# Performance work log

Measured on AMD Instinct MI355X. Metric: run time of the kernel, lower is better.

The kernel has to match this reference:

```python
import jax, jax.numpy as jnp
import numpy as np

TAU = 1.0
EPS_LN = 1e-5


def setup_inputs() -> dict:
    key = jax.random.key(0)
    ks = jax.random.split(key, 6)
    B, D, C, E, H = 32768, 768, 474, 3, 128
    x = jax.random.normal(ks[0], (B, D), dtype=jnp.float32)
    # pre-sampled uniform -> gumbel noise happens in reference; here store standard
    # gumbel noise directly (equivalent distribution to -log(-log(U)))
    u = jax.random.uniform(ks[1], (B, E), dtype=jnp.float32)
    gumbel_noise = -jnp.log(-jnp.log(u + 1e-20) + 1e-20)
    sel_w1 = jax.random.normal(ks[2], (D, H), dtype=jnp.float32) * (1.0 / np.sqrt(D))
    sel_b1 = jnp.zeros((H,), dtype=jnp.float32)
    sel_w2 = jax.random.normal(ks[3], (H, E), dtype=jnp.float32) * (1.0 / np.sqrt(H))
    sel_b2 = jnp.zeros((E,), dtype=jnp.float32)
    ln_gamma = jnp.ones((E, D), dtype=jnp.float32)
    ln_beta = jnp.zeros((E, D), dtype=jnp.float32)
    head_w = jax.random.normal(ks[4], (E, D, C), dtype=jnp.float32) * (1.0 / np.sqrt(D))
    head_b = jnp.zeros((E, C), dtype=jnp.float32)
    return {"x": x, "gumbel_noise": gumbel_noise, "sel_w1": sel_w1, "sel_b1": sel_b1,
            "sel_w2": sel_w2, "sel_b2": sel_b2, "ln_gamma": ln_gamma, "ln_beta": ln_beta,
            "head_w": head_w, "head_b": head_b}


def reference(x, gumbel_noise, sel_w1, sel_b1, sel_w2, sel_b2,
              ln_gamma, ln_beta, head_w, head_b):
    # selector MLP: Linear(768,128) -> ReLU -> Linear(128,3)
    h = jax.nn.relu(x @ sel_w1 + sel_b1)
    logits = h @ sel_w2 + sel_b2                       # [B, 3]

    # hard gumbel-softmax with straight-through estimator
    y = jax.nn.softmax((logits + gumbel_noise) / TAU, axis=-1)
    y_hard = jax.nn.one_hot(jnp.argmax(y, axis=-1), y.shape[-1], dtype=y.dtype)
    selection = jax.lax.stop_gradient(y_hard - y) + y  # [B, 3]

    # 3 expert heads: LayerNorm(768) -> Linear(768,474); dropout is identity (eval)
    mu = jnp.mean(x, axis=-1, keepdims=True)
    var = jnp.mean((x - mu) ** 2, axis=-1, keepdims=True)
    xn = (x - mu) * jax.lax.rsqrt(var + EPS_LN)        # [B, D]
    xs = xn[:, None, :] * ln_gamma[None] + ln_beta[None]   # [B, 3, D]
    outputs = jnp.einsum('bed,edc->bec', xs, head_w) + head_b  # [B, 3, C]

    # mask-and-sum combine
    return jnp.sum(outputs * selection[:, :, None], axis=1)    # [B, C]
```

## Files before the change

### kernel.cpp

```cpp
#include <hip/hip_runtime.h>
#include <hip/hip_bf16.h>
#include <math.h>

#define NB 32768
#define ND 768
#define NC 474
#define NCP 512
#define NE 3
#define NH 128
#define GAP_THR 0.035f
#define XB_OFF 4194304ull

typedef short v8s __attribute__((ext_vector_type(8)));
typedef float v4f __attribute__((ext_vector_type(4)));
typedef unsigned long long u64;

#define GLD16(gp, lp) __builtin_amdgcn_global_load_lds( \
    (const __attribute__((address_space(1))) void*)(gp), \
    (__attribute__((address_space(3))) void*)(lp), 16, 0, 0)

static __device__ __forceinline__ short f2bf(float f) {
    __hip_bfloat16 h = __float2bfloat16(f);
    return *reinterpret_cast<short*>(&h);
}

static __device__ __forceinline__ void vmwait(int n) {
    switch (n) {
    case 0:  asm volatile("s_waitcnt vmcnt(0)"  ::: "memory"); break;
    case 5:  asm volatile("s_waitcnt vmcnt(5)"  ::: "memory"); break;
    case 6:  asm volatile("s_waitcnt vmcnt(6)"  ::: "memory"); break;
    case 12: asm volatile("s_waitcnt vmcnt(12)" ::: "memory"); break;
    default: asm volatile("s_waitcnt vmcnt(10)" ::: "memory"); break;
    }
}

__global__ __launch_bounds__(256) void ln_convert(
    const float* __restrict__ x, float2* __restrict__ murs,
    short* __restrict__ xb, u64* __restrict__ counts,
    float* __restrict__ hz )
{
    const int t = threadIdx.x;
    if (blockIdx.x == 0) {
        if (t == 0) *counts = 0ull;
        #pragma unroll
        for (int i = 0; i < 12; ++i) hz[i * 256 + t] = 0.f;
    }
    const int row = blockIdx.x * 16 + (t >> 4);
    const int q = t & 15;
    const float* xr = x + (size_t)row * ND;
    short* xo = xb + (size_t)row * ND;
    float4 v[12];
    #pragma unroll
    for (int i = 0; i < 12; ++i)
        v[i] = *(const float4*)(xr + (i * 16 + q) * 4);
    float s1 = 0.f, s2 = 0.f;
    #pragma unroll
    for (int i = 0; i < 12; ++i) {
        s1 += v[i].x + v[i].y + v[i].z + v[i].w;
        s2 += v[i].x*v[i].x + v[i].y*v[i].y + v[i].z*v[i].z + v[i].w*v[i].w;
    }
    #pragma unroll
    for (int i = 0; i < 12; ++i) {
        short4 o;
        o.x = f2bf(v[i].x); o.y = f2bf(v[i].y);
        o.z = f2bf(v[i].z); o.w = f2bf(v[i].w);
        *(short4*)(xo + (i * 16 + q) * 4) = o;
    }
    s1 += __shfl_xor(s1, 1); s2 += __shfl_xor(s2, 1);
    s1 += __shfl_xor(s1, 2); s2 += __shfl_xor(s2, 2);
    s1 += __shfl_xor(s1, 4); s2 += __shfl_xor(s2, 4);
    s1 += __shfl_xor(s1, 8); s2 += __shfl_xor(s2, 8);
    if (q == 0) {
        const float mu = s1 * (1.f / 768.f);
        const float var = s2 * (1.f / 768.f) - mu * mu;
        murs[row] = make_float2(mu, rsqrtf(var + 1e-5f));
    }
}

__global__ __launch_bounds__(256) void prep_kernel(
    const float* __restrict__ hw, const float* __restrict__ gamma,
    const float* __restrict__ beta, const float* __restrict__ w1,
    const float* __restrict__ hb,
    short* __restrict__ hwbT, short* __restrict__ w1bT,
    float* __restrict__ hbias, float* __restrict__ csumv)
{
    __shared__ float T[32][72];
    __shared__ float U[32][72];
    const int t = threadIdx.x;
    const int id = blockIdx.x;
    const float* src; short* dst; int stride, ncs; int e = 0, cc, kc;
    bool is_exp = (id < 576);
    if (is_exp) {
        e = id / 192; const int r2 = id % 192; cc = r2 / 24; kc = r2 % 24;
        src = hw + (size_t)e * ND * NC; stride = NC; ncs = NC;
        dst = hwbT + (size_t)e * NCP * ND;
    } else {
        const int j = id - 576; cc = j / 24; kc = j % 24;
        src = w1; stride = NH; ncs = NH; dst = w1bT;
    }
    const int c0 = cc * 64, k0 = kc * 32;
    {
        const int kl = t >> 3, c8 = (t & 7) * 8;
        const float g  = is_exp ? gamma[e * ND + k0 + kl] : 1.f;
        const float bb = is_exp ? beta[e * ND + k0 + kl]  : 0.f;
        #pragma unroll
        for (int j = 0; j < 8; ++j) {
            const int cg = c0 + c8 + j;
            const float v = (cg < ncs) ? src[(size_t)(k0 + kl) * stride + cg] : 0.f;
            T[kl][c8 + j] = v * g;
            U[kl][c8 + j] = v * bb;
        }
    }
    __syncthreads();
    {
        const int cl = t >> 2, q = t & 3;
        const int cg = c0 + cl;
        const int sp = q ^ ((cg >> 1) & 3);
        union { short s[8]; int4 v; } u;
        #pragma unroll
        for (int j = 0; j < 8; ++j) u.s[j] = f2bf(T[q * 8 + j][cl]);
        *(int4*)(dst + (size_t)cg * ND + k0 + sp * 8) = u.v;
    }
    if (is_exp && t < 64) {
        float sg = 0.f, sb = 0.f;
        #pragma unroll 8
        for (int k = 0; k < 32; ++k) {
            sg += T[k][t];
            sb += U[k][t];
        }
        const int c = c0 + t;
        if (kc == 0 && c < NC) sb += hb[e * NC + c];
        atomicAdd(&csumv[e * NCP + c], sg);
        atomicAdd(&hbias[e * NCP + c], sb);
    }
}

__global__ __launch_bounds__(256, 2) void selector_kernel(
    const short* __restrict__ xb, const float* __restrict__ gum,
    const short* __restrict__ w1bT, const float* __restrict__ b1,
    const float* __restrict__ w2, const float* __restrict__ b2,
    u64* __restrict__ counts,
    int* __restrict__ rowlist, int* __restrict__ redolist)
{
    __shared__ __align__(16) char smem[81920];
    short* As = (short*)smem;
    short* Bs = (short*)(smem + 32768);
    float* wpart = (float*)smem;
    float* b1s   = (float*)(smem + 3072);
    float* w2s   = (float*)(smem + 3584);

    const int t = threadIdx.x;
    const int row0 = blockIdx.x * 64;
    const int w = t >> 6, l = t & 63;
    const int g = l >> 4, lm = l & 15;
    const int sr = t >> 2, sq = t & 3;

    const int aslot = sq ^ ((sr >> 1) & 3);
    const short* axsrc = xb + (size_t)(row0 + sr) * ND + aslot * 8;
    const short* bsrc0 = w1bT + (size_t)(w * 32 +  0 + (l >> 2)) * ND + (l & 3) * 8;
    const short* bsrc1 = w1bT + (size_t)(w * 32 + 16 + (l >> 2)) * ND + (l & 3) * 8;
    const int aoff  = __builtin_amdgcn_readfirstlane(w * 512);
    const int boff0 = __builtin_amdgcn_readfirstlane((w * 32 +  0) * 32);
    const int boff1 = __builtin_amdgcn_readfirstlane((w * 32 + 16) * 32);

    v4f acc[4][2];
    #pragma unroll
    for (int i = 0; i < 4; ++i) { acc[i][0] = (v4f)(0.f); acc[i][1] = (v4f)(0.f); }

    #pragma unroll
    for (int s = 0; s < 4; ++s) {
        GLD16(axsrc + s * 32, As + s * 2048 + aoff);
        GLD16(bsrc0 + s * 32, Bs + s * 4096 + boff0);
        GLD16(bsrc1 + s * 32, Bs + s * 4096 + boff1);
    }

    #pragma unroll
    for (int S = 0; S < 12; ++S) {
        if (S <= 9) {
            #pragma unroll
            for (int u = 0; u < 2; ++u) {
                const int j = 2 * S + 4 + u;
                GLD16(axsrc + j * 32, As + (j & 7) * 2048 + aoff);
                GLD16(bsrc0 + j * 32, Bs + (j % 6) * 4096 + boff0);
                GLD16(bsrc1 + j * 32, Bs + (j % 6) * 4096 + boff1);
            }
            vmwait(12);
        } else if (S == 10) {
            vmwait(6);
        } else {
            vmwait(0);
        }
        __builtin_amdgcn_sched_barrier(0);
        __builtin_amdgcn_s_barrier();

        #pragma unroll
        for (int u = 0; u < 2; ++u) {
            const int j = 2 * S + u;
            const short* Aj = As + (j & 7) * 2048;
            const short* Bj = Bs + (j % 6) * 4096;
            v8s af[4];
            #pragma unroll
            for (int mf = 0; mf < 4; ++mf) {
                const int row = mf * 16 + lm;
                af[mf] = *(const v8s*)&Aj[row * 32 + (g ^ ((lm >> 1) & 3)) * 8];
            }
            #pragma unroll
            for (int nf = 0; nf < 2; ++nf) {
                const int cl = w * 32 + nf * 16 + lm;
                const v8s bv = *(const v8s*)&Bj[cl * 32 + (g ^ ((lm >> 1) & 3)) * 8];
                #pragma unroll
                for (int mf = 0; mf < 4; ++mf)
                    acc[mf][nf] = __builtin_amdgcn_mfma_f32_16x16x32_bf16(
                        af[mf], bv, acc[mf][nf], 0, 0, 0);
            }
        }
        asm volatile("s_waitcnt lgkmcnt(0)" ::: "memory");
        __builtin_amdgcn_sched_barrier(0);
    }

    __syncthreads();
    if (t < NH) {
        b1s[t] = b1[t];
        w2s[t*3+0] = w2[t*3+0]; w2s[t*3+1] = w2[t*3+1]; w2s[t*3+2] = w2[t*3+2];
    }
    __syncthreads();

    #pragma unroll
    for (int mf = 0; mf < 4; ++mf) {
        float p[4][3] = {};
        #pragma unroll
        for (int nf = 0; nf < 2; ++nf) {
            const int cl = w * 32 + nf * 16 + lm;
            const float bb = b1s[cl];
            const float wa = w2s[cl*3], wb = w2s[cl*3+1], wc = w2s[cl*3+2];
            #pragma unroll
            for (int r = 0; r < 4; ++r) {
                const float h = fmaxf(acc[mf][nf][r] + bb, 0.f);
                p[r][0] = fmaf(h, wa, p[r][0]);
                p[r][1] = fmaf(h, wb, p[r][1]);
                p[r][2] = fmaf(h, wc, p[r][2]);
            }
        }
        #pragma unroll
        for (int m = 1; m < 16; m <<= 1)
            #pragma unroll
            for (int r = 0; r < 4; ++r) {
                p[r][0] += __shfl_xor(p[r][0], m);
                p[r][1] += __shfl_xor(p[r][1], m);
                p[r][2] += __shfl_xor(p[r][2], m);
            }
        if (lm == 0) {
            #pragma unroll
            for (int r = 0; r < 4; ++r) {
                const int row = mf * 16 + g * 4 + r;
                wpart[(w * 64 + row) * 3 + 0] = p[r][0];
                wpart[(w * 64 + row) * 3 + 1] = p[r][1];
                wpart[(w * 64 + row) * 3 + 2] = p[r][2];
            }
        }
    }
    __syncthreads();

    if (t < 64) {
        const int grow = row0 + l;
        const float z0 = wpart[(0*64+l)*3+0] + wpart[(1*64+l)*3+0]
                       + wpart[(2*64+l)*3+0] + wpart[(3*64+l)*3+0]
                       + b2[0] + gum[grow*3+0];
        const float z1 = wpart[(0*64+l)*3+1] + wpart[(1*64+l)*3+1]
                       + wpart[(2*64+l)*3+1] + wpart[(3*64+l)*3+1]
                       + b2[1] + gum[grow*3+1];
        const float z2 = wpart[(0*64+l)*3+2] + wpart[(1*64+l)*3+2]
                       + wpart[(2*64+l)*3+2] + wpart[(3*64+l)*3+2]
                       + b2[2] + gum[grow*3+2];
        int be = 0; float best = z0;
        if (z1 > best) { best = z1; be = 1; }
        if (z2 > best) { best = z2; be = 2; }
        const float second = (be==0) ? fmaxf(z1,z2) : (be==1) ? fmaxf(z0,z2) : fmaxf(z0,z1);
        if (best - second < GAP_THR) be = 3;

        const u64 m0 = __ballot(be == 0);
        const u64 m1 = __ballot(be == 1);
        const u64 m2 = __ballot(be == 2);
        const u64 m3 = __ballot(be == 3);
        u64 old = 0;
        if (l == 0) {
            const u64 add = (u64)__popcll(m0)
                          | ((u64)__popcll(m1) << 16)
                          | ((u64)__popcll(m2) << 32)
                          | ((u64)__popcll(m3) << 48);
            old = atomicAdd(counts, add);
        }
        const int blo = __shfl((int)(old & 0xFFFFFFFFull), 0);
        const int bhi = __shfl((int)(old >> 32), 0);
        old = ((u64)(unsigned)bhi << 32) | (u64)(unsigned)blo;
        const u64 mym = (be == 0) ? m0 : (be == 1) ? m1 : (be == 2) ? m2 : m3;
        const u64 below = (l == 63) ? 0x7FFFFFFFFFFFFFFFull : ((1ull << l) - 1ull);
        const int rank = __popcll(mym & below);
        const int base = (int)((old >> (16 * be)) & 0xFFFFull);
        const int idx = base + rank;
        if (be < 3) {
            if ((unsigned)idx < NB) rowlist[be * NB + idx] = grow;
        } else {
            if ((unsigned)idx < NB) redolist[idx] = grow;
        }
    }
}

__global__ __launch_bounds__(128) void redo_kernel(
    const float* __restrict__ x, const float* __restrict__ gum,
    const float* __restrict__ w1, const float* __restrict__ b1,
    const float* __restrict__ w2, const float* __restrict__ b2,
    u64* __restrict__ counts, int* __restrict__ rowlist,
    const int* __restrict__ redolist)
{
    const int t = threadIdx.x;
    int n = (int)((*counts >> 48) & 0xFFFFull);
    if (n > NB) n = NB;
    __shared__ float xs[ND];
    __shared__ double red[2][3];
    for (int i = blockIdx.x; i < n; i += gridDim.x) {
        const int row = redolist[i];
        {
            const float4* xp = (const float4*)(x + (size_t)row * ND);
            float4* xsv = (float4*)xs;
            xsv[t] = xp[t];
            if (t < 64) xsv[128 + t] = xp[128 + t];
        }
        __syncthreads();
        double h0 = 0.0, h1 = 0.0, h2 = 0.0, h3 = 0.0;
        double h4 = 0.0, h5 = 0.0, h6 = 0.0, h7 = 0.0;
        #pragma unroll 2
        for (int k = 0; k < ND; k += 8) {
            const float w0 = w1[(size_t)(k+0) * NH + t];
            const float w1v = w1[(size_t)(k+1) * NH + t];
            const float w2v = w1[(size_t)(k+2) * NH + t];
            const float w3 = w1[(size_t)(k+3) * NH + t];
            const float w4 = w1[(size_t)(k+4) * NH + t];
            const float w5 = w1[(size_t)(k+5) * NH + t];
            const float w6 = w1[(size_t)(k+6) * NH + t];
            const float w7 = w1[(size_t)(k+7) * NH + t];
            h0 = fma((double)xs[k+0], (double)w0, h0);
            h1 = fma((double)xs[k+1], (double)w1v, h1);
            h2 = fma((double)xs[k+2], (double)w2v, h2);
            h3 = fma((double)xs[k+3], (double)w3, h3);
            h4 = fma((double)xs[k+4], (double)w4, h4);
            h5 = fma((double)xs[k+5], (double)w5, h5);
            h6 = fma((double)xs[k+6], (double)w6, h6);
            h7 = fma((double)xs[k+7], (double)w7, h7);
        }
        double h = (((h0 + h1) + (h2 + h3)) + ((h4 + h5) + (h6 + h7)))
                 + (double)b1[t];
        h = h > 0.0 ? h : 0.0;
        double p0 = h * (double)w2[t * 3 + 0];
        double p1 = h * (double)w2[t * 3 + 1];
        double p2 = h * (double)w2[t * 3 + 2];
        #pragma unroll
        for (int m = 32; m >= 1; m >>= 1) {
            p0 += __shfl_xor(p0, m);
            p1 += __shfl_xor(p1, m);
            p2 += __shfl_xor(p2, m);
        }
        if ((t & 63) == 0) {
            red[t >> 6][0] = p0; red[t >> 6][1] = p1; red[t >> 6][2] = p2;
        }
        __syncthreads();
        if (t == 0) {
            double best = 0.0; int be = 0;
            #pragma unroll
            for (int e = 0; e < NE; ++e) {
                const double z = red[0][e] + red[1][e] + (double)b2[e]
                               + (double)gum[(size_t)row * 3 + e];
                if (e == 0 || z > best) { best = z; be = e; }
            }
            const u64 old = atomicAdd(counts, 1ull << (16 * be));
            const int pos = (int)((old >> (16 * be)) & 0xFFFFull);
            if ((unsigned)pos < NB) rowlist[be * NB + pos] = row;
        }
        __syncthreads();
    }
}

__global__ __launch_bounds__(256, 3) void head_kernel(
    const short* __restrict__ xb, const float2* __restrict__ murs,
    const short* __restrict__ hwbT, const float* __restrict__ hbias,
    const float* __restrict__ csumv,
    const u64* __restrict__ counts, const int* __restrict__ rowlist,
    float* __restrict__ out)
{
    const int e = blockIdx.z;
    int cnt = (int)((*counts >> (16 * e)) & 0xFFFFull);
    if (cnt > NB) cnt = NB;
    const int rc0 = blockIdx.y * 64;
    if (rc0 >= cnt) return;
    const int n0 = blockIdx.x * 256;

    __shared__ __align__(16) short As[4][2048];
    __shared__ __align__(16) short Bs[2][8192];
    __shared__ float hbs[256], css[256], rs_s[64], rm_s[64];
    __shared__ int rows_s[64];

    const int t = threadIdx.x;
    const int w = t >> 6, l = t & 63;
    const int g = l >> 4, lm = l & 15;
    const int sr = t >> 2, sq = t & 3;

    if (t < 64) {
        const int ri = rc0 + t;
        int rr = (ri < cnt) ? rowlist[e * NB + ri] : -1;
        if (rr >= NB) rr = -1;
        rows_s[t] = rr;
        const float2 mr = (rr >= 0) ? murs[rr] : make_float2(0.f, 0.f);
        rs_s[t] = mr.y;
        rm_s[t] = mr.y * mr.x;
    }
    hbs[t] = (n0 + t < NC) ? hbias[e * NCP + n0 + t] : 0.f;
    css[t] = (n0 + t < NC) ? csumv[e * NCP + n0 + t] : 0.f;

    const int ridx = rc0 + sr;
    int arow = (ridx < cnt) ? rowlist[e * NB + ridx] : 0;
    if ((unsigned)arow >= NB) arow = 0;
    const int aslot = sq ^ ((sr >> 1) & 3);
    const short* axsrc = xb + (size_t)arow * ND + aslot * 8;
    const short* hwe = hwbT + (size_t)e * NCP * ND + (size_t)n0 * ND;
    const int aoff = __builtin_amdgcn_readfirstlane(w * 512);

    v4f acc[4][4];
    #pragma unroll
    for (int i = 0; i < 4; ++i)
        #pragma unroll
        for (int j = 0; j < 4; ++j) acc[i][j] = (v4f)(0.f);

    #pragma unroll
    for (int i = 0; i < 4; ++i) {
        const int crow = w * 64 + i * 16 + (l >> 2);
        const int off = __builtin_amdgcn_readfirstlane((w * 64 + i * 16) * 32);
        GLD16(hwe + (size_t)crow * ND + (l & 3) * 8, &Bs[0][0] + off);
    }
    GLD16(axsrc,      &As[0][0] + aoff);
    GLD16(axsrc + 32, &As[1][0] + aoff);
    __syncthreads();

    #pragma unroll
    for (int ks = 0; ks < 24; ++ks) {
        const int curA = ks & 3;
        const int curB = ks & 1;
        if (ks < 23) {
            #pragma unroll
            for (int i = 0; i < 4; ++i) {
                const int crow = w * 64 + i * 16 + (l >> 2);
                const int off = __builtin_amdgcn_readfirstlane((w * 64 + i * 16) * 32);
                GLD16(hwe + (size_t)crow * ND + (ks + 1) * 32 + (l & 3) * 8,
                      &Bs[(ks + 1) & 1][0] + off);
            }
        }
        if (ks < 22) {
            GLD16(axsrc + (ks + 2) * 32, &As[(ks + 2) & 3][0] + aoff);
        }
        if (ks < 22)       vmwait(6);
        else if (ks == 22) vmwait(5);
        else               vmwait(0);
        __builtin_amdgcn_sched_barrier(0);
        __builtin_amdgcn_s_barrier();

        v8s af[4];
        #pragma unroll
        for (int mf = 0; mf < 4; ++mf) {
            const int row = mf * 16 + lm;
            af[mf] = *(const v8s*)&As[curA][row * 32 + (g ^ ((lm >> 1) & 3)) * 8];
        }
        #pragma unroll
        for (int nf = 0; nf < 4; ++nf) {
            const int cl = w * 64 + nf * 16 + lm;
            const v8s bv = *(const v8s*)&Bs[curB][cl * 32 + (g ^ ((lm >> 1) & 3)) * 8];
            #pragma unroll
            for (int mf = 0; mf < 4; ++mf)
                acc[mf][nf] = __builtin_amdgcn_mfma_f32_16x16x32_bf16(
                    af[mf], bv, acc[mf][nf], 0, 0, 0);
        }
        asm volatile("s_waitcnt lgkmcnt(0)" ::: "memory");
        __builtin_amdgcn_sched_barrier(0);
    }

    #pragma unroll
    for (int mf = 0; mf < 4; ++mf) {
        #pragma unroll
        for (int r = 0; r < 4; ++r) {
            const int rl = mf * 16 + g * 4 + r;
            const int orow = rows_s[rl];
            if (orow < 0) continue;
            const float rs = rs_s[rl], rm = rm_s[rl];
            float* op = out + (size_t)orow * NC;
            #pragma unroll
            for (int nf = 0; nf < 4; ++nf) {
                const int cl = w * 64 + nf * 16 + lm;
                const int c = n0 + cl;
                if (c < NC)
                    op[c] = acc[mf][nf][r] * rs - rm * css[cl] + hbs[cl];
            }
        }
    }
}

extern "C" void kernel_launch(void* const* d_in, const int* in_sizes, int n_in,
                              void* d_out, int out_size, void* d_ws, size_t ws_size,
                              hipStream_t stream) {
    const float* x     = (const float*)d_in[0];
    const float* gum   = (const float*)d_in[1];
    const float* w1    = (const float*)d_in[2];
    const float* b1    = (const float*)d_in[3];
    const float* w2    = (const float*)d_in[4];
    const float* b2    = (const float*)d_in[5];
    const float* gamma = (const float*)d_in[6];
    const float* beta  = (const float*)d_in[7];
    const float* hw    = (const float*)d_in[8];
    const float* hb    = (const float*)d_in[9];
    float* out = (float*)d_out;

    char* ws = (char*)d_ws;
    u64*    counts   = (u64*)ws;
    float2* murs     = (float2*)(ws + 256);
    int*    rowlist  = (int*)(ws + 262400);
    int*    redolist = (int*)(ws + 655616);
    float*  hbias    = (float*)(ws + 786688);
    float*  csumv    = (float*)(ws + 792832);
    short*  w1bT     = (short*)(ws + 798976);
    short*  hwbT     = (short*)(ws + 995584);
    short*  xbg      = (short*)(ws + XB_OFF);

    ln_convert<<<NB / 16, 256, 0, stream>>>(x, murs, xbg, counts, hbias);
    prep_kernel<<<624, 256, 0, stream>>>(hw, gamma, beta, w1, hb,
                                         hwbT, w1bT, hbias, csumv);
    selector_kernel<<<NB / 64, 256, 0, stream>>>(xbg, gum, w1bT, b1, w2, b2,
                                                 counts, rowlist, redolist);
    redo_kernel<<<1024, 128, 0, stream>>>(x, gum, w1, b1, w2, b2,
                                          counts, rowlist, redolist);
    head_kernel<<<dim3(2, NB / 64, NE), 256, 0, stream>>>(
        xbg, murs, hwbT, hbias, csumv, counts, rowlist, out);
}
```

Baseline: 141.5 us.

## Fuse LayerNorm stats and bf16 conversion into selector GEMM prologue

Removes the separate ln_convert pass and has the selector kernel load fp32 x directly. It converts x to bf16 in registers, writes it both to LDS for the MFMA and to global for the head kernel, and accumulates the LayerNorm mean and variance along the way. This drops one full kernel launch and the re-read of the bf16 x copy. In exchange the selector's software pipeline now holds fp32 register prefetches alongside the async LDS loads for w1, with retuned waitcnt values. The hbias zeroing moves to a memset and the counter reset moves into prep_kernel.

```diff
diff --git a/kernel.cpp b/kernel.cpp
--- a/kernel.cpp
+++ b/kernel.cpp
@@ -27,53 +27,11 @@
 static __device__ __forceinline__ void vmwait(int n) {
     switch (n) {
     case 0:  asm volatile("s_waitcnt vmcnt(0)"  ::: "memory"); break;
+    case 4:  asm volatile("s_waitcnt vmcnt(4)"  ::: "memory"); break;
     case 5:  asm volatile("s_waitcnt vmcnt(5)"  ::: "memory"); break;
     case 6:  asm volatile("s_waitcnt vmcnt(6)"  ::: "memory"); break;
-    case 12: asm volatile("s_waitcnt vmcnt(12)" ::: "memory"); break;
+    case 8:  asm volatile("s_waitcnt vmcnt(8)"  ::: "memory"); break;
     default: asm volatile("s_waitcnt vmcnt(10)" ::: "memory"); break;
-    }
-}
-
-__global__ __launch_bounds__(256) void ln_convert(
-    const float* __restrict__ x, float2* __restrict__ murs,
-    short* __restrict__ xb, u64* __restrict__ counts,
-    float* __restrict__ hz )
-{
-    const int t = threadIdx.x;
-    if (blockIdx.x == 0) {
-        if (t == 0) *counts = 0ull;
-        #pragma unroll
-        for (int i = 0; i < 12; ++i) hz[i * 256 + t] = 0.f;
-    }
-    const int row = blockIdx.x * 16 + (t >> 4);
-    const int q = t & 15;
-    const float* xr = x + (size_t)row * ND;
-    short* xo = xb + (size_t)row * ND;
-    float4 v[12];
-    #pragma unroll
-    for (int i = 0; i < 12; ++i)
-        v[i] = *(const float4*)(xr + (i * 16 + q) * 4);
-    float s1 = 0.f, s2 = 0.f;
-    #pragma unroll
-    for (int i = 0; i < 12; ++i) {
-        s1 += v[i].x + v[i].y + v[i].z + v[i].w;
-        s2 += v[i].x*v[i].x + v[i].y*v[i].y + v[i].z*v[i].z + v[i].w*v[i].w;
-    }
-    #pragma unroll
-    for (int i = 0; i < 12; ++i) {
-        short4 o;
-        o.x = f2bf(v[i].x); o.y = f2bf(v[i].y);
-        o.z = f2bf(v[i].z); o.w = f2bf(v[i].w);
-        *(short4*)(xo + (i * 16 + q) * 4) = o;
-    }
-    s1 += __shfl_xor(s1, 1); s2 += __shfl_xor(s2, 1);
-    s1 += __shfl_xor(s1, 2); s2 += __shfl_xor(s2, 2);
-    s1 += __shfl_xor(s1, 4); s2 += __shfl_xor(s2, 4);
-    s1 += __shfl_xor(s1, 8); s2 += __shfl_xor(s2, 8);
-    if (q == 0) {
-        const float mu = s1 * (1.f / 768.f);
-        const float var = s2 * (1.f / 768.f) - mu * mu;
-        murs[row] = make_float2(mu, rsqrtf(var + 1e-5f));
     }
 }
 
@@ -82,12 +40,14 @@
     const float* __restrict__ beta, const float* __restrict__ w1,
     const float* __restrict__ hb,
     short* __restrict__ hwbT, short* __restrict__ w1bT,
-    float* __restrict__ hbias, float* __restrict__ csumv)
+    float* __restrict__ hbias, float* __restrict__ csumv,
+    u64* __restrict__ counts)
 {
     __shared__ float T[32][72];
     __shared__ float U[32][72];
     const int t = threadIdx.x;
     const int id = blockIdx.x;
+    if (id == 0 && t == 0) *counts = 0ull;
     const float* src; short* dst; int stride, ncs; int e = 0, cc, kc;
     bool is_exp = (id < 576);
     if (is_exp) {
@@ -135,10 +95,11 @@
     }
 }
 
-__global__ __launch_bounds__(256, 2) void selector_kernel(
-    const short* __restrict__ xb, const float* __restrict__ gum,
+__global__ __launch_bounds__(256, 2) void lnsel_kernel(
+    const float* __restrict__ x, const float* __restrict__ gum,
     const short* __restrict__ w1bT, const float* __restrict__ b1,
     const float* __restrict__ w2, const float* __restrict__ b2,
+    float2* __restrict__ murs, short* __restrict__ xb,
     u64* __restrict__ counts,
     int* __restrict__ rowlist, int* __restrict__ redolist)
 {
@@ -156,40 +117,76 @@
     const int sr = t >> 2, sq = t & 3;
 
     const int aslot = sq ^ ((sr >> 1) & 3);
-    const short* axsrc = xb + (size_t)(row0 + sr) * ND + aslot * 8;
+    const int awr = sr * 32 + aslot * 8;
+    const float* xrow = x + (size_t)(row0 + sr) * ND + sq * 8;
+    short* xo = xb + (size_t)(row0 + sr) * ND + sq * 8;
     const short* bsrc0 = w1bT + (size_t)(w * 32 +  0 + (l >> 2)) * ND + (l & 3) * 8;
     const short* bsrc1 = w1bT + (size_t)(w * 32 + 16 + (l >> 2)) * ND + (l & 3) * 8;
-    const int aoff  = __builtin_amdgcn_readfirstlane(w * 512);
     const int boff0 = __builtin_amdgcn_readfirstlane((w * 32 +  0) * 32);
     const int boff1 = __builtin_amdgcn_readfirstlane((w * 32 + 16) * 32);
 
     v4f acc[4][2];
     #pragma unroll
     for (int i = 0; i < 4; ++i) { acc[i][0] = (v4f)(0.f); acc[i][1] = (v4f)(0.f); }
-
-    #pragma unroll
-    for (int s = 0; s < 4; ++s) {
-        GLD16(axsrc + s * 32, As + s * 2048 + aoff);
-        GLD16(bsrc0 + s * 32, Bs + s * 4096 + boff0);
-        GLD16(bsrc1 + s * 32, Bs + s * 4096 + boff1);
-    }
+    float s1 = 0.f, s2 = 0.f;
+
+    auto cvst = [&](float4 a, float4 b, int j) {
+        s1 += a.x + a.y + a.z + a.w + b.x + b.y + b.z + b.w;
+        s2 += a.x*a.x + a.y*a.y + a.z*a.z + a.w*a.w
+            + b.x*b.x + b.y*b.y + b.z*b.z + b.w*b.w;
+        v8s v;
+        v[0]=f2bf(a.x); v[1]=f2bf(a.y); v[2]=f2bf(a.z); v[3]=f2bf(a.w);
+        v[4]=f2bf(b.x); v[5]=f2bf(b.y); v[6]=f2bf(b.z); v[7]=f2bf(b.w);
+        *(v8s*)&As[(j & 7) * 2048 + awr] = v;
+        *(v8s*)(xo + j * 32) = v;
+    };
+
+    float4 q0 = *(const float4*)(xrow + 0);
+    float4 q1 = *(const float4*)(xrow + 4);
+    float4 q2 = *(const float4*)(xrow + 32);
+    float4 q3 = *(const float4*)(xrow + 36);
+    float4 cA0 = *(const float4*)(xrow + 64);
+    float4 cA1 = *(const float4*)(xrow + 68);
+    float4 cB0 = *(const float4*)(xrow + 96);
+    float4 cB1 = *(const float4*)(xrow + 100);
+    #pragma unroll
+    for (int j = 0; j < 4; ++j) {
+        GLD16(bsrc0 + j * 32, Bs + j * 4096 + boff0);
+        GLD16(bsrc1 + j * 32, Bs + j * 4096 + boff1);
+    }
+    __builtin_amdgcn_sched_barrier(0);
+    vmwait(8);
+    __builtin_amdgcn_sched_barrier(0);
+    cvst(q0, q1, 0);
+    cvst(q2, q3, 1);
 
     #pragma unroll
     for (int S = 0; S < 12; ++S) {
+        float4 pA0, pA1, pB0, pB1;
         if (S <= 9) {
-            #pragma unroll
-            for (int u = 0; u < 2; ++u) {
-                const int j = 2 * S + 4 + u;
-                GLD16(axsrc + j * 32, As + (j & 7) * 2048 + aoff);
-                GLD16(bsrc0 + j * 32, Bs + (j % 6) * 4096 + boff0);
-                GLD16(bsrc1 + j * 32, Bs + (j % 6) * 4096 + boff1);
-            }
-            vmwait(12);
+            const int j4 = 2 * S + 4;
+            pA0 = *(const float4*)(xrow + j4 * 32);
+            pA1 = *(const float4*)(xrow + j4 * 32 + 4);
+            pB0 = *(const float4*)(xrow + j4 * 32 + 32);
+            pB1 = *(const float4*)(xrow + j4 * 32 + 36);
+            GLD16(bsrc0 + j4 * 32,        Bs + (j4 % 6) * 4096 + boff0);
+            GLD16(bsrc1 + j4 * 32,        Bs + (j4 % 6) * 4096 + boff1);
+            GLD16(bsrc0 + (j4 + 1) * 32,  Bs + ((j4 + 1) % 6) * 4096 + boff0);
+            GLD16(bsrc1 + (j4 + 1) * 32,  Bs + ((j4 + 1) % 6) * 4096 + boff1);
+            __builtin_amdgcn_sched_barrier(0);
+            vmwait(10);
         } else if (S == 10) {
             vmwait(6);
         } else {
-            vmwait(0);
-        }
+            vmwait(4);
+        }
+        __builtin_amdgcn_sched_barrier(0);
+        if (S <= 10) {
+            cvst(cA0, cA1, 2 * S + 2);
+            cvst(cB0, cB1, 2 * S + 3);
+        }
+        if (S <= 9) { cA0 = pA0; cA1 = pA1; cB0 = pB0; cB1 = pB1; }
+        asm volatile("s_waitcnt lgkmcnt(0)" ::: "memory");
         __builtin_amdgcn_sched_barrier(0);
         __builtin_amdgcn_s_barrier();
 
@@ -216,6 +213,18 @@
         }
         asm volatile("s_waitcnt lgkmcnt(0)" ::: "memory");
         __builtin_amdgcn_sched_barrier(0);
+    }
+
+    {
+        float r1 = s1 + __shfl_xor(s1, 1);
+        float r2 = s2 + __shfl_xor(s2, 1);
+        r1 += __shfl_xor(r1, 2);
+        r2 += __shfl_xor(r2, 2);
+        if (sq == 0) {
+            const float mu = r1 * (1.f / 768.f);
+            const float var = r2 * (1.f / 768.f) - mu * mu;
+            murs[row0 + sr] = make_float2(mu, rsqrtf(var + 1e-5f));
+        }
     }
 
     __syncthreads();
@@ -527,11 +536,12 @@
     short*  hwbT     = (short*)(ws + 995584);
     short*  xbg      = (short*)(ws + XB_OFF);
 
-    ln_convert<<<NB / 16, 256, 0, stream>>>(x, murs, xbg, counts, hbias);
+    hipMemsetAsync(hbias, 0, 12288, stream);
     prep_kernel<<<624, 256, 0, stream>>>(hw, gamma, beta, w1, hb,
-                                         hwbT, w1bT, hbias, csumv);
-    selector_kernel<<<NB / 64, 256, 0, stream>>>(xbg, gum, w1bT, b1, w2, b2,
-                                                 counts, rowlist, redolist);
+                                         hwbT, w1bT, hbias, csumv, counts);
+    lnsel_kernel<<<NB / 64, 256, 0, stream>>>(x, gum, w1bT, b1, w2, b2,
+                                              murs, xbg, counts,
+                                              rowlist, redolist);
     redo_kernel<<<1024, 128, 0, stream>>>(x, gum, w1, b1, w2, b2,
                                           counts, rowlist, redolist);
     head_kernel<<<dim3(2, NB / 64, NE), 256, 0, stream>>>(
```

New measurement: 134.2 us (median of 2 runs). 1.05x faster.
